# Kernel optimization log

Measured on AMD Instinct MI355X. Metric: run time of the kernel, lower is better.

## Reference

```python
import jax, jax.numpy as jnp
import numpy as np

TD_DENOM = 3600.0  # td_upper - td_lower
SD_DENOM = 1000.0  # sd_upper - sd_lower

B, T, E, H = 64, 256, 512, 512
V, NB = 50000, 128


def setup_inputs() -> dict:
    key = jax.random.key(0)
    ks = jax.random.split(key, 16)
    s = 0.02
    return {
        'loc_seq': jax.random.randint(ks[0], (B, T), 0, V),
        'td_upper_seq': jax.random.randint(ks[1], (B, T), 0, NB),
        'td_lower_seq': jax.random.randint(ks[2], (B, T), 0, NB),
        'sd_upper_seq': jax.random.randint(ks[3], (B, T), 0, NB),
        'sd_lower_seq': jax.random.randint(ks[4], (B, T), 0, NB),
        'valid_lengths': jax.random.randint(ks[5], (B,), 1, T + 1),
        'loc_emb': jax.random.normal(ks[6], (V, E), jnp.float32) * s,
        't_up_emb': jax.random.normal(ks[7], (NB, E), jnp.float32) * s,
        't_lo_emb': jax.random.normal(ks[8], (NB, E), jnp.float32) * s,
        's_up_emb': jax.random.normal(ks[9], (NB, E), jnp.float32) * s,
        's_lo_emb': jax.random.normal(ks[10], (NB, E), jnp.float32) * s,
        'Wt': jax.random.normal(ks[11], (E, 3 * H), jnp.float32) * s,
        'Ws': jax.random.normal(ks[12], (E, 3 * H), jnp.float32) * s,
        'Wi': jax.random.normal(ks[13], (E, 4 * H), jnp.float32) * s,
        'bi': jnp.zeros((4 * H,), jnp.float32),
        'Wh': jax.random.normal(ks[14], (H, 4 * H), jnp.float32) * s,
    }


def reference(loc_seq, td_upper_seq, td_lower_seq, sd_upper_seq, sd_lower_seq,
              valid_lengths, loc_emb, t_up_emb, t_lo_emb, s_up_emb, s_lo_emb,
              Wt, Ws, Wi, bi, Wh):
    Bs, Ts = loc_seq.shape
    Hs = Wh.shape[0]
    x = loc_emb[loc_seq]                                            # (B,T,E)
    q = (t_up_emb[td_upper_seq] + t_lo_emb[td_lower_seq]) / TD_DENOM
    sp = (s_up_emb[sd_upper_seq] + s_lo_emb[sd_lower_seq]) / SD_DENOM
    # first_step zeroes q and s
    mask = (jnp.arange(Ts) > 0).astype(x.dtype)[None, :, None]
    q = q * mask
    sp = sp * mask
    Fp = jnp.einsum('bte,ef->btf', q, Wt) + jnp.einsum('bte,ef->btf', sp, Ws)  # (B,T,3H)
    xp = jnp.einsum('bte,ef->btf', x, Wi) + bi                                  # (B,T,4H)

    def step(carry, xs):
        h, c = carry
        xpt, Ft = xs
        tmp = xpt + h @ Wh
        i_t, f_t, o_t, g_t = jnp.split(tmp, 4, axis=1)
        i_F, f_F, o_F = jnp.split(Ft, 3, axis=1)
        i_t = jax.nn.sigmoid(i_t + i_F)
        f_t = jax.nn.sigmoid(f_t + f_F)
        o_t = jax.nn.sigmoid(o_t + o_F)
        g_t = jnp.tanh(g_t)
        c = f_t * c + i_t * g_t
        h = o_t * jnp.tanh(c)
        return (h, c), (h, c)

    h0 = jnp.zeros((Bs, Hs), x.dtype)
    c0 = jnp.zeros((Bs, Hs), x.dtype)
    (hT, cT), (hs, cs) = jax.lax.scan(
        step, (h0, c0), (xp.transpose(1, 0, 2), Fp.transpose(1, 0, 2)))
    all_h = hs.transpose(1, 0, 2)  # (B,T,H)
    all_c = cs.transpose(1, 0, 2)
    # original prepends the final hidden, then selects index (valid_length+1)-1
    all_h_full = jnp.concatenate([hT[:, None], all_h], axis=1)  # (B,T+1,H)
    all_c_full = jnp.concatenate([cT[:, None], all_c], axis=1)
    b_idx = jnp.arange(Bs)
    last_h = all_h_full[b_idx, valid_lengths]
    last_c = all_c_full[b_idx, valid_lengths]
    return (all_h, last_h, last_c)
```

## Files before the change

### kernel.cpp

```cpp
#include <hip/hip_runtime.h>
#include <stdint.h>

#define A_CAT_OFF  0ull
#define WCT_OFF    50331648ull
#define WHR_OFF    56623104ull
#define G_OFF      58720256ull
#define HBUF_OFF   125829120ull
#define WS_NEED    126091264ull

typedef short bf16x8 __attribute__((ext_vector_type(8)));
typedef float f32x4  __attribute__((ext_vector_type(4)));

__device__ __forceinline__ unsigned short f2bf(float f) {
  union { float f; uint32_t u; } v; v.f = f;
  uint32_t u = v.u;
  u += 0x7FFFu + ((u >> 16) & 1u);
  return (unsigned short)(u >> 16);
}
__device__ __forceinline__ float bf2f(unsigned short h) {
  union { uint32_t u; float f; } v; v.u = ((uint32_t)h) << 16;
  return v.f;
}
__device__ __forceinline__ float u2f(uint32_t u) {
  union { uint32_t u; float f; } v; v.u = u; return v.f;
}
__device__ __forceinline__ uint32_t f2u(float f) {
  union { float f; uint32_t u; } v; v.f = f; return v.u;
}
__device__ __forceinline__ float fsigmoid(float x) { return 1.0f / (1.0f + __expf(-x)); }
__device__ __forceinline__ float ftanh(float x) {
  float e = __expf(2.0f * x);
  return 1.0f - 2.0f / (e + 1.0f);
}
__device__ __forceinline__ uint4 pack8(const unsigned short* v) {
  uint4 r;
  r.x = (uint32_t)v[0] | ((uint32_t)v[1] << 16);
  r.y = (uint32_t)v[2] | ((uint32_t)v[3] << 16);
  r.z = (uint32_t)v[4] | ((uint32_t)v[5] << 16);
  r.w = (uint32_t)v[6] | ((uint32_t)v[7] << 16);
  return r;
}

#define GLOAD_LDS16(GP, LP)                                                   \
  __builtin_amdgcn_global_load_lds(                                          \
      (const __attribute__((address_space(1))) uint32_t*)(GP),               \
      (__attribute__((address_space(3))) uint32_t*)(LP), 16, 0, 0)

__global__ __launch_bounds__(256) void k_prep(
    const float* __restrict__ Wi, const float* __restrict__ Wt,
    const float* __restrict__ Ws, const float* __restrict__ Wh,
    uint8_t* ws) {
  int id = blockIdx.x * 256 + threadIdx.x;
  if (id < 393216) {
    int n  = id & 2047;
    int k0 = (id >> 11) << 3;
    unsigned short v[8];
#pragma unroll
    for (int j = 0; j < 8; ++j) {
      int k = k0 + j;
      float x;
      if (k < 512)       x = Wi[k * 2048 + n];
      else if (k < 1024) x = (n < 1536) ? Wt[(k - 512) * 1536 + n] : 0.0f;
      else               x = (n < 1536) ? Ws[(k - 1024) * 1536 + n] : 0.0f;
      v[j] = f2bf(x);
    }
    size_t off = WCT_OFF + (size_t)n * 3072 +
                 (size_t)(((uint32_t)k0 * 2u) ^ (((uint32_t)n & 7u) << 4));
    *(uint4*)(ws + off) = pack8(v);
  } else if (id < 524288) {
    int id2 = id - 393216;
    int cc  = id2 & 2047;
    int k0  = (id2 >> 11) << 3;
    int col = ((cc >> 5) & 3) * 512 + (cc >> 7) * 32 + (cc & 31);
    unsigned short v[8];
#pragma unroll
    for (int j = 0; j < 8; ++j) v[j] = f2bf(Wh[(size_t)(k0 + j) * 2048 + col]);
    size_t off = WHR_OFF + (size_t)cc * 1024 +
                 (size_t)(((uint32_t)k0 * 2u) ^ (((uint32_t)cc & 7u) << 4));
    *(uint4*)(ws + off) = pack8(v);
  } else if (id < 532480) {
    uint4 z; z.x = z.y = z.z = z.w = 0u;
    *(uint4*)(ws + HBUF_OFF + (size_t)(id - 524288) * 16) = z;
  } else {
    uint4 z; z.x = z.y = z.z = z.w = 1u;
    *(uint4*)(ws + HBUF_OFF + 131072ull + (size_t)(id - 532480) * 16) = z;
  }
}

__global__ __launch_bounds__(192) void k_gather(
    const int* __restrict__ loc, const int* __restrict__ tdu,
    const int* __restrict__ tdl, const int* __restrict__ sdu,
    const int* __restrict__ sdl,
    const float* __restrict__ loc_emb, const float* __restrict__ tup,
    const float* __restrict__ tlo, const float* __restrict__ sup,
    const float* __restrict__ slo, uint8_t* ws) {
  int m  = blockIdx.x;
  int t  = m & 255;
  int k0 = threadIdx.x << 3;
  float vals[8];
  if (k0 < 512) {
    const float* s = loc_emb + (size_t)loc[m] * 512 + k0;
#pragma unroll
    for (int j = 0; j < 8; ++j) vals[j] = s[j];
  } else if (k0 < 1024) {
    int e = k0 - 512;
    const float* a = tup + (size_t)tdu[m] * 512 + e;
    const float* b = tlo + (size_t)tdl[m] * 512 + e;
    float sc = (t > 0) ? (1.0f / 3600.0f) : 0.0f;
#pragma unroll
    for (int j = 0; j < 8; ++j) vals[j] = (a[j] + b[j]) * sc;
  } else {
    int e = k0 - 1024;
    const float* a = sup + (size_t)sdu[m] * 512 + e;
    const float* b = slo + (size_t)sdl[m] * 512 + e;
    float sc = (t > 0) ? (1.0f / 1000.0f) : 0.0f;
#pragma unroll
    for (int j = 0; j < 8; ++j) vals[j] = (a[j] + b[j]) * sc;
  }
  unsigned short v[8];
#pragma unroll
  for (int j = 0; j < 8; ++j) v[j] = f2bf(vals[j]);
  size_t off = A_CAT_OFF + (size_t)m * 3072 +
               (size_t)(((uint32_t)k0 * 2u) ^ (((uint32_t)m & 7u) << 4));
  *(uint4*)(ws + off) = pack8(v);
}

__global__ __launch_bounds__(256) void k_gemm(uint8_t* ws,
                                              const float* __restrict__ bi) {
  __shared__ uint8_t A_lds[16384];
  __shared__ uint8_t B_lds[16384];
  const uint8_t* Acat = ws + A_CAT_OFF;
  const uint8_t* Wct  = ws + WCT_OFF;
  uint8_t* Gp = ws + G_OFF;
  int tid = threadIdx.x;
  int lane = tid & 63, wave = tid >> 6;
  int wm = wave >> 1, wn = wave & 1;
  int tile_m = blockIdx.x >> 4, tile_n = blockIdx.x & 15;

  f32x4 acc[4][4];
#pragma unroll
  for (int m = 0; m < 4; ++m)
#pragma unroll
    for (int n = 0; n < 4; ++n) acc[m][n] = f32x4{0.f, 0.f, 0.f, 0.f};

  for (int kb = 0; kb < 1536; kb += 64) {
#pragma unroll
    for (int i = 0; i < 4; ++i) {
      int lidx = i * 256 + tid;
      int row = lidx >> 3, ch = lidx & 7;
      GLOAD_LDS16(Acat + (size_t)(tile_m * 128 + row) * 3072 + kb * 2 + ch * 16,
                  A_lds + (i * 256 + wave * 64) * 16);
    }
#pragma unroll
    for (int i = 0; i < 4; ++i) {
      int lidx = i * 256 + tid;
      int row = lidx >> 3, ch = lidx & 7;
      GLOAD_LDS16(Wct + (size_t)(tile_n * 128 + row) * 3072 + kb * 2 + ch * 16,
                  B_lds + (i * 256 + wave * 64) * 16);
    }
    __syncthreads();
#pragma unroll
    for (int kk = 0; kk < 2; ++kk) {
      int koff = kk * 64 + ((lane >> 4) << 4);
      bf16x8 af[4], bfr[4];
#pragma unroll
      for (int m = 0; m < 4; ++m) {
        int row = wm * 64 + m * 16 + (lane & 15);
        af[m] = *(const bf16x8*)(A_lds + row * 128 + (koff ^ ((row & 7) << 4)));
      }
#pragma unroll
      for (int n = 0; n < 4; ++n) {
        int row = wn * 64 + n * 16 + (lane & 15);
        bfr[n] = *(const bf16x8*)(B_lds + row * 128 + (koff ^ ((row & 7) << 4)));
      }
#pragma unroll
      for (int m = 0; m < 4; ++m)
#pragma unroll
        for (int n = 0; n < 4; ++n)
          acc[m][n] = __builtin_amdgcn_mfma_f32_16x16x32_bf16(af[m], bfr[n],
                                                              acc[m][n], 0, 0, 0);
    }
    __syncthreads();
  }
  int lr = lane >> 4, lc = lane & 15;
#pragma unroll
  for (int n = 0; n < 4; ++n) {
    int gcol = tile_n * 128 + wn * 64 + n * 16 + lc;
    float bv = bi[gcol];
#pragma unroll
    for (int m = 0; m < 4; ++m) {
      int growb = tile_m * 128 + wm * 64 + m * 16 + lr * 4;
#pragma unroll
      for (int q = 0; q < 4; ++q) {
        int grow = growb + q;
        float v = acc[m][n][q] + bv;
        size_t gi = ((size_t)(grow & 255) * 64 + (size_t)(grow >> 8)) * 2048 + gcol;
        *(unsigned short*)(Gp + gi * 2) = f2bf(v);
      }
    }
  }
}

__global__ __launch_bounds__(512) void k_recur(uint8_t* ws,
                                               const int* __restrict__ vlen,
                                               float* __restrict__ out) {
  int bid = blockIdx.x;
  if ((bid & 7) >= 4) return;
  int r = bid & 7, c = bid >> 3;

  extern __shared__ uint8_t smem[];
  uint8_t* Wh_lds = smem;
  uint8_t* h_lds  = smem + 131072;
  float*   tmp    = (float*)(smem + 147456);

  int tid = threadIdx.x;
  int lane = tid & 63, wave = tid >> 6;

  const uint8_t* Gp  = ws + G_OFF;
  const uint8_t* Whr = ws + WHR_OFF;

  {
    const uint8_t* src = Whr + (size_t)c * 131072;
#pragma unroll
    for (int i = 0; i < 16; ++i) {
      int cb = i * 512 + wave * 64;
      GLOAD_LDS16(src + (size_t)(cb + lane) * 16, Wh_lds + (size_t)cb * 16);
    }
  }

  int wv = tid & 255;
  int bh = tid >> 8;
  int gb = tid >> 5;
  int d  = tid & 31;
  int gbatch = r * 16 + gb;
  int vl = vlen[gbatch];
  float cr = 0.0f;
  bool fb = false;
  float* outH  = out;
  float* outLH = out + 8388608;
  float* outLC = out + 8421376;

  const uint8_t* gthr = Gp + ((size_t)(r * 16 + gb) * 2048 +
                              (size_t)(c * 32 + d)) * 2;
  unsigned short gc0, gc1, gc2, gc3;
  gc0 = *(const unsigned short*)(gthr);
  gc1 = *(const unsigned short*)(gthr + 1024);
  gc2 = *(const unsigned short*)(gthr + 2048);
  gc3 = *(const unsigned short*)(gthr + 3072);

  __syncthreads();

  for (int t = 0; t < 256; ++t) {
    uint64_t x[8];
    {
      const uint8_t* hb = ws + HBUF_OFF + (size_t)(t & 1) * 131072 +
                          (size_t)r * 32768;
      uint32_t expect = (uint32_t)((t >> 1) & 1);
      int passes = 0;
      for (;;) {
        if (!fb) {
#pragma unroll
          for (int i = 0; i < 8; ++i) {
            const void* p = hb + (size_t)(bh * 8 + i) * 2048 + (size_t)wv * 8;
            asm volatile("global_load_dwordx2 %0, %1, off sc0"
                         : "=v"(x[i]) : "v"(p));
          }
          asm volatile("s_waitcnt vmcnt(0)" ::: "memory");
          __builtin_amdgcn_sched_barrier(0);
        } else {
#pragma unroll
          for (int i = 0; i < 8; ++i)
            x[i] = __hip_atomic_load(
                (const uint64_t*)(hb + (size_t)(bh * 8 + i) * 2048 +
                                  (size_t)wv * 8),
                __ATOMIC_RELAXED, __HIP_MEMORY_SCOPE_AGENT);
        }
        uint32_t bad = 0;
#pragma unroll
        for (int i = 0; i < 8; ++i) {
          uint32_t lo = (uint32_t)x[i], hi = (uint32_t)(x[i] >> 32);
          bad |= ((lo ^ expect) & 1u) | ((hi ^ expect) & 1u);
        }
        if (!bad) break;
        if (++passes > 64) fb = true;
      }
    }
    unsigned short gn0, gn1, gn2, gn3;
    {
      int tn = (t + 1) & 255;
      const uint8_t* gp = gthr + (size_t)tn * 262144;
      gn0 = *(const unsigned short*)(gp);
      gn1 = *(const unsigned short*)(gp + 1024);
      gn2 = *(const unsigned short*)(gp + 2048);
      gn3 = *(const unsigned short*)(gp + 3072);
    }
#pragma unroll
    for (int i = 0; i < 8; ++i) {
      int bl = bh * 8 + i;
      uint32_t lo = (uint32_t)x[i], hi = (uint32_t)(x[i] >> 32);
      uint32_t pk = (uint32_t)f2bf(u2f(lo)) | ((uint32_t)f2bf(u2f(hi)) << 16);
      *(uint32_t*)(h_lds + bl * 1024 + ((wv * 4) ^ ((bl & 7) << 4))) = pk;
    }
    __syncthreads();

    f32x4 acc = f32x4{0.f, 0.f, 0.f, 0.f};
    {
      int lrow = lane & 15;
      int g16 = (lane >> 4) << 4;
      int rb = wave * 16 + lrow;
      int swz = (lrow & 7) << 4;
#pragma unroll
      for (int kk = 0; kk < 16; ++kk) {
        int ko = kk * 64 + g16;
        bf16x8 a = *(const bf16x8*)(h_lds + lrow * 1024 + (ko ^ swz));
        bf16x8 b = *(const bf16x8*)(Wh_lds + (size_t)rb * 1024 + (ko ^ swz));
        acc = __builtin_amdgcn_mfma_f32_16x16x32_bf16(a, b, acc, 0, 0, 0);
      }
    }
    {
      int colb = wave * 16 + (lane & 15);
      int xorv = ((lane >> 4) & 1) << 4;
      int rowd = (lane >> 4) << 2;
#pragma unroll
      for (int q = 0; q < 4; ++q)
        tmp[(rowd + q) * 128 + (colb ^ xorv)] = acc[q];
    }
    __syncthreads();

    float hval, cval;
    {
      int xo = ((gb >> 2) & 1) << 4;
      float ip = tmp[gb * 128 + ((d)      ^ xo)] + bf2f(gc0);
      float fp = tmp[gb * 128 + ((d + 32) ^ xo)] + bf2f(gc1);
      float op = tmp[gb * 128 + ((d + 64) ^ xo)] + bf2f(gc2);
      float gp = tmp[gb * 128 + ((d + 96) ^ xo)] + bf2f(gc3);
      float ig = fsigmoid(ip), fg = fsigmoid(fp), og = fsigmoid(op);
      float gt = ftanh(gp);
      cval = fg * cr + ig * gt;
      cr = cval;
      hval = og * ftanh(cval);
    }
    {
      uint32_t wtag = (uint32_t)(((t + 1) >> 1) & 1);
      uint32_t w0 = (f2u(hval) & ~1u) | wtag;
      uint32_t* hw = (uint32_t*)(ws + HBUF_OFF + (size_t)((t + 1) & 1) * 131072);
      uint32_t* pub = &hw[(size_t)gbatch * 512 + (size_t)(c * 32 + d)];
      asm volatile("global_store_dword %0, %1, off"
                   :: "v"(pub), "v"(w0) : "memory");
      __hip_atomic_store(pub, w0, __ATOMIC_RELAXED, __HIP_MEMORY_SCOPE_AGENT);
    }
    outH[((size_t)gbatch * 256 + (size_t)t) * 512 + (size_t)(c * 32 + d)] = hval;
    if (t == vl - 1) {
      size_t lb = (size_t)gbatch * 512 + (size_t)(c * 32 + d);
      outLH[lb] = hval;
      outLC[lb] = cval;
    }
    gc0 = gn0; gc1 = gn1; gc2 = gn2; gc3 = gn3;
  }
}

extern "C" void kernel_launch(void* const* d_in, const int* in_sizes, int n_in,
                              void* d_out, int out_size, void* d_ws, size_t ws_size,
                              hipStream_t stream) {
  const int*   loc     = (const int*)d_in[0];
  const int*   tdu     = (const int*)d_in[1];
  const int*   tdl     = (const int*)d_in[2];
  const int*   sdu     = (const int*)d_in[3];
  const int*   sdl     = (const int*)d_in[4];
  const int*   vlen    = (const int*)d_in[5];
  const float* loc_emb = (const float*)d_in[6];
  const float* tup     = (const float*)d_in[7];
  const float* tlo     = (const float*)d_in[8];
  const float* sup     = (const float*)d_in[9];
  const float* slo     = (const float*)d_in[10];
  const float* Wt      = (const float*)d_in[11];
  const float* Ws      = (const float*)d_in[12];
  const float* Wi      = (const float*)d_in[13];
  const float* bi      = (const float*)d_in[14];
  const float* Wh      = (const float*)d_in[15];
  uint8_t* ws = (uint8_t*)d_ws;
  float* out = (float*)d_out;

  if (ws_size < WS_NEED) return;

  (void)hipFuncSetAttribute((const void*)k_recur,
                            hipFuncAttributeMaxDynamicSharedMemorySize, 155648);

  k_prep  <<<2112, 256, 0, stream>>>(Wi, Wt, Ws, Wh, ws);
  k_gather<<<16384, 192, 0, stream>>>(loc, tdu, tdl, sdu, sdl,
                                      loc_emb, tup, tlo, sup, slo, ws);
  k_gemm  <<<2048, 256, 0, stream>>>(ws, bi);
  k_recur <<<128, 512, 155648, stream>>>(ws, vlen, out);
}
```

Before: 1.215 ms.

## Use per-block sentinel counters for recurrence sync and keep Wh in registers

The recurrent kernel stops polling tag bits embedded in every h value and instead polls one step counter per column block. Each block publishes its counter after a vmcnt wait and a barrier. The Wh slice moves from LDS into per-lane register fragments (16 bf16x8), which shrinks LDS and removes B-operand LDS reads from the MFMA loop. The output store of h is deferred by one step, and the G gate values are loaded directly instead of prefetched. This risks higher register pressure and adds an extra barrier and memory fence per step.

Measured after the change: 1.297 ms. +6.7%, slower.

```diff
diff --git a/kernel.cpp b/kernel.cpp
--- a/kernel.cpp
+++ b/kernel.cpp
@@ -6,7 +6,8 @@
 #define WHR_OFF    56623104ull
 #define G_OFF      58720256ull
 #define HBUF_OFF   125829120ull
-#define WS_NEED    126091264ull
+#define SENT_OFF   126091264ull
+#define WS_NEED    126091520ull
 
 typedef short bf16x8 __attribute__((ext_vector_type(8)));
 typedef float f32x4  __attribute__((ext_vector_type(4)));
@@ -75,15 +76,13 @@
     unsigned short v[8];
 #pragma unroll
     for (int j = 0; j < 8; ++j) v[j] = f2bf(Wh[(size_t)(k0 + j) * 2048 + col]);
-    size_t off = WHR_OFF + (size_t)cc * 1024 +
-                 (size_t)(((uint32_t)k0 * 2u) ^ (((uint32_t)cc & 7u) << 4));
-    *(uint4*)(ws + off) = pack8(v);
+    *(uint4*)(ws + WHR_OFF + (size_t)cc * 1024 + (size_t)k0 * 2) = pack8(v);
   } else if (id < 532480) {
     uint4 z; z.x = z.y = z.z = z.w = 0u;
     *(uint4*)(ws + HBUF_OFF + (size_t)(id - 524288) * 16) = z;
-  } else {
-    uint4 z; z.x = z.y = z.z = z.w = 1u;
-    *(uint4*)(ws + HBUF_OFF + 131072ull + (size_t)(id - 532480) * 16) = z;
+  } else if (id < 532496) {
+    uint4 z; z.x = z.y = z.z = z.w = 0u;
+    *(uint4*)(ws + SENT_OFF + (size_t)(id - 532480) * 16) = z;
   }
 }
 
@@ -201,105 +200,116 @@
   }
 }
 
-__global__ __launch_bounds__(512) void k_recur(uint8_t* ws,
-                                               const int* __restrict__ vlen,
-                                               float* __restrict__ out) {
+__global__ __launch_bounds__(512, 2) void k_recur(uint8_t* ws,
+                                                  const int* __restrict__ vlen,
+                                                  float* __restrict__ out) {
   int bid = blockIdx.x;
   if ((bid & 7) >= 4) return;
   int r = bid & 7, c = bid >> 3;
 
   extern __shared__ uint8_t smem[];
-  uint8_t* Wh_lds = smem;
-  uint8_t* h_lds  = smem + 131072;
-  float*   tmp    = (float*)(smem + 147456);
+  uint8_t* h_lds = smem;
+  float*   tmp   = (float*)(smem + 16384);
 
   int tid = threadIdx.x;
   int lane = tid & 63, wave = tid >> 6;
 
   const uint8_t* Gp  = ws + G_OFF;
   const uint8_t* Whr = ws + WHR_OFF;
-
+  uint32_t* sent = (uint32_t*)(ws + SENT_OFF) + r * 16;
+
+  bf16x8 Bfrag[16];
   {
-    const uint8_t* src = Whr + (size_t)c * 131072;
-#pragma unroll
-    for (int i = 0; i < 16; ++i) {
-      int cb = i * 512 + wave * 64;
-      GLOAD_LDS16(src + (size_t)(cb + lane) * 16, Wh_lds + (size_t)cb * 16);
-    }
-  }
-
-  int wv = tid & 255;
-  int bh = tid >> 8;
-  int gb = tid >> 5;
-  int d  = tid & 31;
+    int cc = c * 128 + wave * 16 + (lane & 15);
+    const uint8_t* wb = Whr + (size_t)cc * 1024 + ((lane >> 4) << 4);
+#pragma unroll
+    for (int kk = 0; kk < 16; ++kk)
+      Bfrag[kk] = *(const bf16x8*)(wb + kk * 64);
+  }
+
+  int gb = tid >> 5, d = tid & 31;
   int gbatch = r * 16 + gb;
   int vl = vlen[gbatch];
-  float cr = 0.0f;
+  float cr = 0.0f, hprev = 0.0f, cprev = 0.0f;
   bool fb = false;
+
+  int hb_b = 2 * wave + (lane >> 5);
+  int hb_byte = (lane & 31) * 64;
+
   float* outH  = out;
   float* outLH = out + 8388608;
   float* outLC = out + 8421376;
 
-  const uint8_t* gthr = Gp + ((size_t)(r * 16 + gb) * 2048 +
-                              (size_t)(c * 32 + d)) * 2;
-  unsigned short gc0, gc1, gc2, gc3;
-  gc0 = *(const unsigned short*)(gthr);
-  gc1 = *(const unsigned short*)(gthr + 1024);
-  gc2 = *(const unsigned short*)(gthr + 2048);
-  gc3 = *(const unsigned short*)(gthr + 3072);
-
   __syncthreads();
 
   for (int t = 0; t < 256; ++t) {
-    uint64_t x[8];
-    {
-      const uint8_t* hb = ws + HBUF_OFF + (size_t)(t & 1) * 131072 +
-                          (size_t)r * 32768;
-      uint32_t expect = (uint32_t)((t >> 1) & 1);
+    {
+      const uint32_t* sp = sent + (lane & 15);
       int passes = 0;
       for (;;) {
+        uint32_t sv;
         if (!fb) {
-#pragma unroll
-          for (int i = 0; i < 8; ++i) {
-            const void* p = hb + (size_t)(bh * 8 + i) * 2048 + (size_t)wv * 8;
-            asm volatile("global_load_dwordx2 %0, %1, off sc0"
-                         : "=v"(x[i]) : "v"(p));
-          }
-          asm volatile("s_waitcnt vmcnt(0)" ::: "memory");
+          asm volatile("global_load_dword %0, %1, off sc0\n\t"
+                       "s_waitcnt vmcnt(0)"
+                       : "=v"(sv) : "v"(sp) : "memory");
           __builtin_amdgcn_sched_barrier(0);
         } else {
-#pragma unroll
-          for (int i = 0; i < 8; ++i)
-            x[i] = __hip_atomic_load(
-                (const uint64_t*)(hb + (size_t)(bh * 8 + i) * 2048 +
-                                  (size_t)wv * 8),
-                __ATOMIC_RELAXED, __HIP_MEMORY_SCOPE_AGENT);
+          sv = __hip_atomic_load(sp, __ATOMIC_RELAXED, __HIP_MEMORY_SCOPE_AGENT);
         }
-        uint32_t bad = 0;
+        if (__ballot(sv >= (uint32_t)t) == ~0ULL) break;
+        if (++passes > 64) fb = true;
+      }
+    }
+    uint64_t x[8];
+    {
+      const uint8_t* hb = ws + HBUF_OFF + (size_t)(t & 1) * 131072 +
+                          (size_t)(r * 16 + hb_b) * 2048 + hb_byte;
+      if (!fb) {
 #pragma unroll
         for (int i = 0; i < 8; ++i) {
-          uint32_t lo = (uint32_t)x[i], hi = (uint32_t)(x[i] >> 32);
-          bad |= ((lo ^ expect) & 1u) | ((hi ^ expect) & 1u);
+          const void* p = hb + i * 8;
+          asm volatile("global_load_dwordx2 %0, %1, off sc0"
+                       : "=v"(x[i]) : "v"(p) : "memory");
         }
-        if (!bad) break;
-        if (++passes > 64) fb = true;
-      }
-    }
-    unsigned short gn0, gn1, gn2, gn3;
-    {
-      int tn = (t + 1) & 255;
-      const uint8_t* gp = gthr + (size_t)tn * 262144;
-      gn0 = *(const unsigned short*)(gp);
-      gn1 = *(const unsigned short*)(gp + 1024);
-      gn2 = *(const unsigned short*)(gp + 2048);
-      gn3 = *(const unsigned short*)(gp + 3072);
-    }
-#pragma unroll
-    for (int i = 0; i < 8; ++i) {
-      int bl = bh * 8 + i;
-      uint32_t lo = (uint32_t)x[i], hi = (uint32_t)(x[i] >> 32);
-      uint32_t pk = (uint32_t)f2bf(u2f(lo)) | ((uint32_t)f2bf(u2f(hi)) << 16);
-      *(uint32_t*)(h_lds + bl * 1024 + ((wv * 4) ^ ((bl & 7) << 4))) = pk;
+        asm volatile("s_waitcnt vmcnt(0)" ::: "memory");
+        __builtin_amdgcn_sched_barrier(0);
+      } else {
+#pragma unroll
+        for (int i = 0; i < 8; ++i)
+          x[i] = __hip_atomic_load((const uint64_t*)(hb + i * 8),
+                                   __ATOMIC_RELAXED, __HIP_MEMORY_SCOPE_AGENT);
+      }
+    }
+    unsigned short gv0, gv1, gv2, gv3;
+    {
+      const uint8_t* gp = Gp + (size_t)(t * 64 + gbatch) * 4096 +
+                          (size_t)(c * 64 + d * 2);
+      gv0 = *(const unsigned short*)(gp);
+      gv1 = *(const unsigned short*)(gp + 1024);
+      gv2 = *(const unsigned short*)(gp + 2048);
+      gv3 = *(const unsigned short*)(gp + 3072);
+    }
+    if (t > 0) {
+      outH[((size_t)gbatch * 256 + (size_t)(t - 1)) * 512 + (size_t)(c * 32 + d)] = hprev;
+      if (t - 1 == vl - 1) {
+        size_t lb = (size_t)gbatch * 512 + (size_t)(c * 32 + d);
+        outLH[lb] = hprev;
+        outLC[lb] = cprev;
+      }
+    }
+    {
+      uint32_t w[8];
+#pragma unroll
+      for (int i = 0; i < 8; ++i) {
+        uint32_t lo = (uint32_t)x[i], hi = (uint32_t)(x[i] >> 32);
+        w[i] = (uint32_t)f2bf(u2f(lo)) | ((uint32_t)f2bf(u2f(hi)) << 16);
+      }
+      int base = hb_b * 1024 + (lane & 31) * 32;
+      int swz = (hb_b & 7) << 4;
+      uint4 v0; v0.x = w[0]; v0.y = w[1]; v0.z = w[2]; v0.w = w[3];
+      uint4 v1; v1.x = w[4]; v1.y = w[5]; v1.z = w[6]; v1.w = w[7];
+      *(uint4*)(h_lds + (base ^ swz)) = v0;
+      *(uint4*)(h_lds + ((base + 16) ^ swz)) = v1;
     }
     __syncthreads();
 
@@ -307,33 +317,29 @@
     {
       int lrow = lane & 15;
       int g16 = (lane >> 4) << 4;
-      int rb = wave * 16 + lrow;
-      int swz = (lrow & 7) << 4;
+      int aswz = (lrow & 7) << 4;
 #pragma unroll
       for (int kk = 0; kk < 16; ++kk) {
-        int ko = kk * 64 + g16;
-        bf16x8 a = *(const bf16x8*)(h_lds + lrow * 1024 + (ko ^ swz));
-        bf16x8 b = *(const bf16x8*)(Wh_lds + (size_t)rb * 1024 + (ko ^ swz));
-        acc = __builtin_amdgcn_mfma_f32_16x16x32_bf16(a, b, acc, 0, 0, 0);
+        bf16x8 a = *(const bf16x8*)(h_lds + lrow * 1024 + ((kk * 64 + g16) ^ aswz));
+        acc = __builtin_amdgcn_mfma_f32_16x16x32_bf16(a, Bfrag[kk], acc, 0, 0, 0);
       }
     }
     {
       int colb = wave * 16 + (lane & 15);
-      int xorv = ((lane >> 4) & 1) << 4;
       int rowd = (lane >> 4) << 2;
 #pragma unroll
       for (int q = 0; q < 4; ++q)
-        tmp[(rowd + q) * 128 + (colb ^ xorv)] = acc[q];
+        tmp[(rowd + q) * 132 + colb] = acc[q];
     }
     __syncthreads();
 
     float hval, cval;
     {
-      int xo = ((gb >> 2) & 1) << 4;
-      float ip = tmp[gb * 128 + ((d)      ^ xo)] + bf2f(gc0);
-      float fp = tmp[gb * 128 + ((d + 32) ^ xo)] + bf2f(gc1);
-      float op = tmp[gb * 128 + ((d + 64) ^ xo)] + bf2f(gc2);
-      float gp = tmp[gb * 128 + ((d + 96) ^ xo)] + bf2f(gc3);
+      int tb = gb * 132 + d;
+      float ip = tmp[tb]      + bf2f(gv0);
+      float fp = tmp[tb + 32] + bf2f(gv1);
+      float op = tmp[tb + 64] + bf2f(gv2);
+      float gp = tmp[tb + 96] + bf2f(gv3);
       float ig = fsigmoid(ip), fg = fsigmoid(fp), og = fsigmoid(op);
       float gt = ftanh(gp);
       cval = fg * cr + ig * gt;
@@ -341,21 +347,27 @@
       hval = og * ftanh(cval);
     }
     {
-      uint32_t wtag = (uint32_t)(((t + 1) >> 1) & 1);
-      uint32_t w0 = (f2u(hval) & ~1u) | wtag;
-      uint32_t* hw = (uint32_t*)(ws + HBUF_OFF + (size_t)((t + 1) & 1) * 131072);
-      uint32_t* pub = &hw[(size_t)gbatch * 512 + (size_t)(c * 32 + d)];
-      asm volatile("global_store_dword %0, %1, off"
-                   :: "v"(pub), "v"(w0) : "memory");
-      __hip_atomic_store(pub, w0, __ATOMIC_RELAXED, __HIP_MEMORY_SCOPE_AGENT);
-    }
-    outH[((size_t)gbatch * 256 + (size_t)t) * 512 + (size_t)(c * 32 + d)] = hval;
-    if (t == vl - 1) {
-      size_t lb = (size_t)gbatch * 512 + (size_t)(c * 32 + d);
-      outLH[lb] = hval;
-      outLC[lb] = cval;
-    }
-    gc0 = gn0; gc1 = gn1; gc2 = gn2; gc3 = gn3;
+      uint32_t hw = f2u(hval);
+      uint32_t* pub = (uint32_t*)(ws + HBUF_OFF + (size_t)((t + 1) & 1) * 131072 +
+                                  (size_t)gbatch * 2048 + (size_t)(c * 32 + d) * 4);
+      asm volatile("global_store_dword %0, %1, off" :: "v"(pub), "v"(hw) : "memory");
+      __hip_atomic_store(pub, hw, __ATOMIC_RELAXED, __HIP_MEMORY_SCOPE_AGENT);
+    }
+    hprev = hval; cprev = cval;
+    asm volatile("s_waitcnt vmcnt(0)" ::: "memory");
+    __syncthreads();
+    if (tid == 0) {
+      uint32_t sval = (uint32_t)(t + 1);
+      uint32_t* sc = sent + c;
+      asm volatile("global_store_dword %0, %1, off" :: "v"(sc), "v"(sval) : "memory");
+      __hip_atomic_store(sc, sval, __ATOMIC_RELAXED, __HIP_MEMORY_SCOPE_AGENT);
+    }
+  }
+  outH[((size_t)gbatch * 256 + 255) * 512 + (size_t)(c * 32 + d)] = hprev;
+  if (vl == 256) {
+    size_t lb = (size_t)gbatch * 512 + (size_t)(c * 32 + d);
+    outLH[lb] = hprev;
+    outLC[lb] = cprev;
   }
 }
 
@@ -384,11 +396,11 @@
   if (ws_size < WS_NEED) return;
 
   (void)hipFuncSetAttribute((const void*)k_recur,
-                            hipFuncAttributeMaxDynamicSharedMemorySize, 155648);
-
-  k_prep  <<<2112, 256, 0, stream>>>(Wi, Wt, Ws, Wh, ws);
+                            hipFuncAttributeMaxDynamicSharedMemorySize, 98304);
+
+  k_prep  <<<2081, 256, 0, stream>>>(Wi, Wt, Ws, Wh, ws);
   k_gather<<<16384, 192, 0, stream>>>(loc, tdu, tdl, sdu, sdl,
                                       loc_emb, tup, tlo, sup, slo, ws);
   k_gemm  <<<2048, 256, 0, stream>>>(ws, bi);
-  k_recur <<<128, 512, 155648, stream>>>(ws, vlen, out);
-}
+  k_recur <<<128, 512, 98304, stream>>>(ws, vlen, out);
+}
```
